# Kernel optimization log

Measured on AMD Instinct MI355X. Metric: run time of the kernel, lower is better.

Reference implementation:

```python
import jax, jax.numpy as jnp
import numpy as np

N_ATOMS = 50000
N_INT = 800000  # interactions (i,j pairs)
N_IN = 128
NFM = 128
LOG2 = float(np.log(2.0))


def ssp(a):
    # shifted softplus: log(0.5*exp(x) + 0.5) = softplus(x) - log(2)
    return jax.nn.softplus(a) - LOG2


def setup_inputs() -> dict:
    key = jax.random.key(0)
    ks = jax.random.split(key, 12)
    s = 1.0 / np.sqrt(NFM)
    inp = {
        "x": jax.random.normal(ks[0], (N_ATOMS, NFM), dtype=jnp.float32),
        "dijk": jax.random.normal(ks[1], (N_INT, N_IN), dtype=jnp.float32),
        "idx_j": jax.random.randint(ks[2], (N_INT,), 0, N_ATOMS),
        "seg_i": jnp.sort(jax.random.randint(ks[3], (N_INT,), 0, N_ATOMS)),
        "seg_j": jnp.arange(N_INT),
        "seg_i_sum": jnp.ones((N_ATOMS,), dtype=jnp.int64 if jax.config.jax_enable_x64 else jnp.int32),
        # filternet params
        "W_f1": jax.random.normal(ks[4], (N_IN, NFM), dtype=jnp.float32) * s,
        "b_f1": jnp.zeros((NFM,), dtype=jnp.float32),
        "W_f2": jax.random.normal(ks[5], (NFM, NFM), dtype=jnp.float32) * s,
        "b_f2": jnp.zeros((NFM,), dtype=jnp.float32),
        # cfconv params
        "W_in2fac": jax.random.normal(ks[6], (NFM, NFM), dtype=jnp.float32) * s,
        "W_fac2out": jax.random.normal(ks[7], (NFM, NFM), dtype=jnp.float32) * s,
        "b_fac2out": jnp.zeros((NFM,), dtype=jnp.float32),
        # output dense params
        "W_dense": jax.random.normal(ks[8], (NFM, NFM), dtype=jnp.float32) * s,
        "b_dense": jnp.zeros((NFM,), dtype=jnp.float32),
    }
    return inp


def reference(x, dijk, idx_j, seg_i, seg_j, seg_i_sum,
              W_f1, b_f1, W_f2, b_f2,
              W_in2fac, W_fac2out, b_fac2out,
              W_dense, b_dense):
    n_atoms = x.shape[0]
    n_int = idx_j.shape[0]
    # CFnetFilter: two shifted-softplus dense layers over triples, pool -> per-interaction filters
    h = ssp(dijk @ W_f1 + b_f1)                                   # [T, nFM]
    w_ijk = ssp(h @ W_f2 + b_f2)                                  # [T, nFM]
    w_ij = jax.ops.segment_sum(w_ijk, seg_j, num_segments=n_int)  # [E, nFM]
    # CFConv: in2fac dense, gather neighbor features, filter-multiply, segment-sum pool, fac2out dense
    f = x @ W_in2fac                                              # [N, nFM]
    f_j = f[idx_j]                                                # gather -> [E, nFM]
    wf = w_ij * f_j                                               # [E, nFM]
    conv = jax.ops.segment_sum(wf, seg_i, num_segments=n_atoms)   # [N, nFM]
    c = ssp(conv @ W_fac2out + b_fac2out)                         # [N, nFM]
    # output dense (no activation) + residual
    v = c @ W_dense + b_dense                                     # [N, nFM]
    y = x + v
    return (y, v)
```

## Files before the change

kernel.cpp:

```cpp
#include <hip/hip_runtime.h>
#include <hip/hip_bf16.h>
#include <stdint.h>

#define NATOMS 50000
#define NINT   800000
#define NFM    128
#define VOFF   (NATOMS*NFM)
#define NBLK   (NINT/256)
#define CBLK   (NINT/128)

typedef __bf16 bf16x8 __attribute__((ext_vector_type(8)));
typedef float  f32x4  __attribute__((ext_vector_type(4)));
typedef unsigned short u16;
typedef u16 u16x8 __attribute__((ext_vector_type(8)));
typedef u16 u16x4 __attribute__((ext_vector_type(4)));

__device__ __forceinline__ u16 f2b(float f){
  __bf16 h = (__bf16)f;
  return __builtin_bit_cast(u16, h);
}
__device__ __forceinline__ float b2f(u16 v){
  return (float)__builtin_bit_cast(__bf16, v);
}

__device__ __forceinline__ float sspf(float x){
  float t = exp2f(-fabsf(x) * 1.44269504088896f);
  return fmaxf(x, 0.0f) + 0.69314718055995f * log2f(1.0f + t) - 0.69314718055995f;
}

__global__ void zero_k(float4* __restrict__ p, int n4){
  int i = blockIdx.x * blockDim.x + threadIdx.x;
  int stride = gridDim.x * blockDim.x;
  float4 z = make_float4(0.f, 0.f, 0.f, 0.f);
  for (; i < n4; i += stride) p[i] = z;
}

__global__ void prep_weights_k(const float* __restrict__ w0, const float* __restrict__ w1,
                               const float* __restrict__ w2, const float* __restrict__ w3,
                               const float* __restrict__ w4, u16* __restrict__ wt){
  const float* srcs[5] = {w0, w1, w2, w3, w4};
  const float* src = srcs[blockIdx.x];
  u16* dst = wt + (size_t)blockIdx.x * NFM * NFM;
  for (int i = threadIdx.x; i < NFM*NFM; i += blockDim.x){
    int n = i >> 7, k = i & 127;
    dst[i] = f2b(src[k*NFM + n]);
  }
}

__device__ __forceinline__ void stage_inp(u16* lsA, const float* __restrict__ src,
                                          int base_row, int n_total, int t){
  #pragma unroll
  for (int pp = 0; pp < 8; ++pp){
    int id  = pp*512 + t;
    int row = id >> 4, c = id & 15;
    int grow = base_row + row;
    float4 v0 = make_float4(0.f,0.f,0.f,0.f), v1 = v0;
    if (grow < n_total){
      const float4* gp = reinterpret_cast<const float4*>(src + (size_t)grow*NFM + c*8);
      v0 = gp[0]; v1 = gp[1];
    }
    u16x8 pk;
    pk[0]=f2b(v0.x); pk[1]=f2b(v0.y); pk[2]=f2b(v0.z); pk[3]=f2b(v0.w);
    pk[4]=f2b(v1.x); pk[5]=f2b(v1.y); pk[6]=f2b(v1.z); pk[7]=f2b(v1.w);
    int byte = row*256 + ((c*16) ^ ((row & 7) << 4));
    *reinterpret_cast<u16x8*>(reinterpret_cast<char*>(lsA) + byte) = pk;
  }
}

__device__ __forceinline__ void stage_w(u16* lsW, const u16* __restrict__ wt, int t){
  #pragma unroll
  for (int pp = 0; pp < 4; ++pp){
    int id = pp*512 + t;
    int n = id >> 4, c = id & 15;
    u16x8 v = *reinterpret_cast<const u16x8*>(wt + n*NFM + c*8);
    int byte = n*256 + ((c*16) ^ ((n & 7) << 4));
    *reinterpret_cast<u16x8*>(reinterpret_cast<char*>(lsW) + byte) = v;
  }
}

__device__ __forceinline__ void gemm_tile(const u16* lsA, const u16* lsW,
                                          int wrow, int l15, int lk, f32x4 acc[2][8]){
  #pragma unroll
  for (int ks = 0; ks < 4; ++ks){
    int kb2 = (ks*32 + lk*8) * 2;
    int r0 = wrow + l15, r1 = wrow + 16 + l15;
    bf16x8 a0 = *reinterpret_cast<const bf16x8*>(reinterpret_cast<const char*>(lsA) + r0*256 + (kb2 ^ ((r0 & 7) << 4)));
    bf16x8 a1 = *reinterpret_cast<const bf16x8*>(reinterpret_cast<const char*>(lsA) + r1*256 + (kb2 ^ ((r1 & 7) << 4)));
    #pragma unroll
    for (int ni = 0; ni < 8; ++ni){
      int n = ni*16 + l15;
      bf16x8 b = *reinterpret_cast<const bf16x8*>(reinterpret_cast<const char*>(lsW) + n*256 + (kb2 ^ ((n & 7) << 4)));
      acc[0][ni] = __builtin_amdgcn_mfma_f32_16x16x32_bf16(a0, b, acc[0][ni], 0, 0, 0);
      acc[1][ni] = __builtin_amdgcn_mfma_f32_16x16x32_bf16(a1, b, acc[1][ni], 0, 0, 0);
    }
  }
}

__global__ __launch_bounds__(512, 2) void in2fac_k(const float* __restrict__ x,
                                                   const u16* __restrict__ wt,
                                                   u16* __restrict__ f_g){
  __shared__ u16 lsA[256*128];
  __shared__ u16 lsW[128*128];
  int t = threadIdx.x;
  int B0 = blockIdx.x * 256;
  stage_inp(lsA, x, B0, NATOMS, t);
  stage_w(lsW, wt, t);
  __syncthreads();
  int wid = t >> 6, lane = t & 63, l15 = lane & 15, lk = lane >> 4;
  int wrow = wid * 32;
  f32x4 acc[2][8] = {};
  gemm_tile(lsA, lsW, wrow, l15, lk, acc);
  #pragma unroll
  for (int mi = 0; mi < 2; ++mi)
    #pragma unroll
    for (int ni = 0; ni < 8; ++ni)
      #pragma unroll
      for (int j = 0; j < 4; ++j){
        int grow = B0 + wrow + mi*16 + lk*4 + j;
        if (grow < NATOMS) f_g[(size_t)grow*NFM + ni*16 + l15] = f2b(acc[mi][ni][j]);
      }
}

__global__ __launch_bounds__(512) __attribute__((amdgpu_waves_per_eu(4, 4)))
void filter_k(const float* __restrict__ dijk,
              const float* __restrict__ b_f1, const float* __restrict__ b_f2,
              const u16* __restrict__ wt1, const u16* __restrict__ wt2,
              u16* __restrict__ w_g){
  __shared__ u16 lsW[2*128*128];
  __shared__ u16 lsS[8192];
  int t = threadIdx.x;
  int B0 = blockIdx.x * 256;
  int wid = t >> 6, lane = t & 63, l15 = lane & 15, lk = lane >> 4;

  f32x4 araw[16];
  {
    const float* abase = dijk + (size_t)(B0 + wid*32 + l15) * NFM;
    #pragma unroll
    for (int mi = 0; mi < 2; ++mi)
      #pragma unroll
      for (int ks = 0; ks < 4; ++ks){
        const f32x4* gp = reinterpret_cast<const f32x4*>(abase + mi*16*NFM + ks*32 + lk*8);
        araw[(mi*4+ks)*2+0] = __builtin_nontemporal_load(gp);
        araw[(mi*4+ks)*2+1] = __builtin_nontemporal_load(gp+1);
      }
  }

  stage_w(lsW, wt1, t);
  stage_w(lsW + 16384, wt2, t);

  float bias1[8], bias2[8];
  #pragma unroll
  for (int ni = 0; ni < 8; ++ni){ bias1[ni] = b_f1[ni*16 + l15]; bias2[ni] = b_f2[ni*16 + l15]; }

  bf16x8 aa[2][4];
  #pragma unroll
  for (int mi = 0; mi < 2; ++mi)
    #pragma unroll
    for (int ks = 0; ks < 4; ++ks){
      f32x4 v0 = araw[(mi*4+ks)*2], v1 = araw[(mi*4+ks)*2+1];
      u16x8 pk;
      pk[0]=f2b(v0[0]); pk[1]=f2b(v0[1]); pk[2]=f2b(v0[2]); pk[3]=f2b(v0[3]);
      pk[4]=f2b(v1[0]); pk[5]=f2b(v1[1]); pk[6]=f2b(v1[2]); pk[7]=f2b(v1[3]);
      aa[mi][ks] = __builtin_bit_cast(bf16x8, pk);
    }

  __syncthreads();

  char* wbase = reinterpret_cast<char*>(lsS) + wid*2048;
  const char* lsW1b = reinterpret_cast<const char*>(lsW);
  const char* lsW2b = reinterpret_cast<const char*>(lsW + 16384);

  #pragma unroll
  for (int mi = 0; mi < 2; ++mi){
    f32x4 acc[8] = {};
    #pragma unroll
    for (int ks = 0; ks < 4; ++ks){
      int kb2 = (ks*32 + lk*8) * 2;
      #pragma unroll
      for (int ni = 0; ni < 8; ++ni){
        int n = ni*16 + l15;
        bf16x8 b = *reinterpret_cast<const bf16x8*>(lsW1b + n*256 + (kb2 ^ ((n & 7) << 4)));
        acc[ni] = __builtin_amdgcn_mfma_f32_16x16x32_bf16(aa[mi][ks], b, acc[ni], 0, 0, 0);
      }
    }
    bf16x8 h[4];
    #pragma unroll
    for (int p = 0; p < 2; ++p){
      #pragma unroll
      for (int nn = 0; nn < 4; ++nn){
        int col = nn*16 + l15;
        #pragma unroll
        for (int j = 0; j < 4; ++j){
          int r = lk*4 + j;
          *reinterpret_cast<u16*>(wbase + r*128 + ((col*2) ^ ((r & 7) << 4))) = f2b(sspf(acc[p*4+nn][j] + bias1[p*4+nn]));
        }
      }
      #pragma unroll
      for (int ksl = 0; ksl < 2; ++ksl)
        h[p*2+ksl] = *reinterpret_cast<const bf16x8*>(wbase + l15*128 + ((ksl*64 + lk*16) ^ ((l15 & 7) << 4)));
    }
    #pragma unroll
    for (int p = 0; p < 2; ++p){
      f32x4 acc2[4] = {};
      #pragma unroll
      for (int ks = 0; ks < 4; ++ks){
        int kb2 = (ks*32 + lk*8) * 2;
        #pragma unroll
        for (int nn = 0; nn < 4; ++nn){
          int n = (p*4 + nn)*16 + l15;
          bf16x8 b = *reinterpret_cast<const bf16x8*>(lsW2b + n*256 + (kb2 ^ ((n & 7) << 4)));
          acc2[nn] = __builtin_amdgcn_mfma_f32_16x16x32_bf16(h[ks], b, acc2[nn], 0, 0, 0);
        }
      }
      #pragma unroll
      for (int nn = 0; nn < 4; ++nn){
        int col = nn*16 + l15;
        #pragma unroll
        for (int j = 0; j < 4; ++j){
          int r = lk*4 + j;
          *reinterpret_cast<u16*>(wbase + r*128 + ((col*2) ^ ((r & 7) << 4))) = f2b(sspf(acc2[nn][j] + bias2[p*4+nn]));
        }
      }
      int row16 = lane & 15, chunk = lane >> 4;
      u16x8 v0 = *reinterpret_cast<const u16x8*>(wbase + row16*128 + ((chunk*32) ^ ((row16 & 7) << 4)));
      u16x8 v1 = *reinterpret_cast<const u16x8*>(wbase + row16*128 + ((chunk*32 + 16) ^ ((row16 & 7) << 4)));
      u16* gdst = w_g + (size_t)(B0 + wid*32 + mi*16 + row16)*NFM + p*64 + chunk*16;
      *reinterpret_cast<u16x8*>(gdst)     = v0;
      *reinterpret_cast<u16x8*>(gdst + 8) = v1;
    }
  }
}

__global__ __launch_bounds__(512) void conv_k(const int* __restrict__ idx_j,
    const int* __restrict__ seg_i, const u16* __restrict__ f_g,
    const u16* __restrict__ w_g, float* __restrict__ conv){
  __shared__ int lsSeg[128];
  __shared__ int lsIdx[128];
  int t = threadIdx.x;
  int B0 = blockIdx.x * 128;
  if (t < 128){ lsSeg[t] = seg_i[B0 + t]; lsIdx[t] = idx_j[B0 + t]; }
  __syncthreads();
  int c2 = t & 63, q = t >> 6;
  int qs = q*16, qe = qs + 16;
  int gc = c2*2;
  int prevseg = (qs > 0) ? lsSeg[qs-1] : (B0 > 0 ? seg_i[B0-1] : -1);
  int nextseg = (qe < 128) ? lsSeg[qe] : (B0 + 128 < NINT ? seg_i[B0+128] : -1);
  const u16* wtile = w_g + (size_t)B0*NFM;
  float s0 = 0.f, s1 = 0.f;
  int cur = lsSeg[qs], rs = qs;
  #pragma unroll 8
  for (int r = qs; r < qe; ++r){
    int sg = lsSeg[r];
    uint32_t wv = __builtin_nontemporal_load(reinterpret_cast<const uint32_t*>(wtile + (size_t)r*NFM + gc));
    uint32_t fv = *reinterpret_cast<const uint32_t*>(f_g + (size_t)lsIdx[r]*NFM + gc);
    if (sg != cur){
      float* dp = conv + (size_t)cur*NFM + gc;
      if (rs == qs && prevseg == cur){ atomicAdd(dp, s0); atomicAdd(dp+1, s1); }
      else { *reinterpret_cast<float2*>(dp) = make_float2(s0, s1); }
      cur = sg; rs = r; s0 = 0.f; s1 = 0.f;
    }
    s0 = fmaf(b2f((u16)(wv & 0xffff)), b2f((u16)(fv & 0xffff)), s0);
    s1 = fmaf(b2f((u16)(wv >> 16)),   b2f((u16)(fv >> 16)),   s1);
  }
  float* dp = conv + (size_t)cur*NFM + gc;
  if ((rs == qs && prevseg == cur) || nextseg == cur){ atomicAdd(dp, s0); atomicAdd(dp+1, s1); }
  else { *reinterpret_cast<float2*>(dp) = make_float2(s0, s1); }
}

__global__ __launch_bounds__(512, 2) void out_k(const float* __restrict__ conv,
    const float* __restrict__ x, const u16* __restrict__ wt3, const u16* __restrict__ wt4,
    const float* __restrict__ b3, const float* __restrict__ b4, float* __restrict__ out){
  __shared__ u16 lsA[256*128];
  __shared__ u16 lsW1[128*128];
  __shared__ u16 lsW2[128*128];
  int t = threadIdx.x;
  int B0 = blockIdx.x * 256;
  stage_inp(lsA, conv, B0, NATOMS, t);
  stage_w(lsW1, wt3, t);
  stage_w(lsW2, wt4, t);
  __syncthreads();
  int wid = t >> 6, lane = t & 63, l15 = lane & 15, lk = lane >> 4;
  int wrow = wid * 32;
  float bias3[8], bias4[8];
  #pragma unroll
  for (int ni = 0; ni < 8; ++ni){ bias3[ni] = b3[ni*16 + l15]; bias4[ni] = b4[ni*16 + l15]; }

  f32x4 acc1[2][8] = {};
  gemm_tile(lsA, lsW1, wrow, l15, lk, acc1);
  #pragma unroll
  for (int mi = 0; mi < 2; ++mi)
    #pragma unroll
    for (int ni = 0; ni < 8; ++ni)
      #pragma unroll
      for (int j = 0; j < 4; ++j){
        int row = wrow + mi*16 + lk*4 + j;
        int col = ni*16 + l15;
        u16 hb = f2b(sspf(acc1[mi][ni][j] + bias3[ni]));
        int byte = row*256 + ((col*2) ^ ((row & 7) << 4));
        *reinterpret_cast<u16*>(reinterpret_cast<char*>(lsA) + byte) = hb;
      }

  f32x4 acc2[2][8] = {};
  gemm_tile(lsA, lsW2, wrow, l15, lk, acc2);
  #pragma unroll
  for (int mi = 0; mi < 2; ++mi)
    #pragma unroll
    for (int ni = 0; ni < 8; ++ni)
      #pragma unroll
      for (int j = 0; j < 4; ++j){
        int grow = B0 + wrow + mi*16 + lk*4 + j;
        if (grow < NATOMS){
          int col = ni*16 + l15;
          float v = acc2[mi][ni][j] + bias4[ni];
          float yv = x[(size_t)grow*NFM + col] + v;
          out[(size_t)grow*NFM + col] = yv;
          out[(size_t)VOFF + (size_t)grow*NFM + col] = v;
        }
      }
}

extern "C" void kernel_launch(void* const* d_in, const int* in_sizes, int n_in,
                              void* d_out, int out_size, void* d_ws, size_t ws_size,
                              hipStream_t stream){
  const float* x        = (const float*)d_in[0];
  const float* dijk     = (const float*)d_in[1];
  const int*   idx_j    = (const int*)d_in[2];
  const int*   seg_i    = (const int*)d_in[3];
  const float* W_f1     = (const float*)d_in[6];
  const float* b_f1     = (const float*)d_in[7];
  const float* W_f2     = (const float*)d_in[8];
  const float* b_f2     = (const float*)d_in[9];
  const float* W_in2fac = (const float*)d_in[10];
  const float* W_fac2o  = (const float*)d_in[11];
  const float* b_fac2o  = (const float*)d_in[12];
  const float* W_dense  = (const float*)d_in[13];
  const float* b_dense  = (const float*)d_in[14];
  float* out = (float*)d_out;

  char* ws = (char*)d_ws;
  u16*   f_g  = (u16*)ws;
  float* conv = (float*)(ws + 12800000);
  u16*   wt   = (u16*)(ws + 38400000);
  u16*   w_g  = (u16*)(ws + 38600000);
  u16* wt1 = wt;
  u16* wt2 = wt + 16384;
  u16* wt5 = wt + 2*16384;
  u16* wt3 = wt + 3*16384;
  u16* wt4 = wt + 4*16384;

  prep_weights_k<<<5, 256, 0, stream>>>(W_f1, W_f2, W_in2fac, W_fac2o, W_dense, wt);
  zero_k<<<2048, 256, 0, stream>>>(reinterpret_cast<float4*>(conv), NATOMS*NFM/4);
  in2fac_k<<<(NATOMS + 255)/256, 512, 0, stream>>>(x, wt5, f_g);
  filter_k<<<NBLK, 512, 0, stream>>>(dijk, b_f1, b_f2, wt1, wt2, w_g);
  conv_k<<<CBLK, 512, 0, stream>>>(idx_j, seg_i, f_g, w_g, conv);
  out_k<<<(NATOMS + 255)/256, 512, 0, stream>>>(conv, x, wt3, wt4, b_fac2o, b_dense, out);
}
```

Before: 328.1 us.

## Widen conv blocks to 512 rows with one column per thread, simplify softplus

The conv kernel now gives each block 512 interactions, each thread one column over 128 consecutive rows instead of two columns over 16 rows. Longer per-thread row runs should mean fewer boundary atomics and fewer blocks. The cost is narrower 2-byte loads instead of 4-byte ones and less parallelism per row. The shifted softplus also drops its numerically stable form for a direct log(1+exp(x)), which is cheaper but can overflow for large positive inputs.

```diff
diff --git a/kernel.cpp b/kernel.cpp
--- a/kernel.cpp
+++ b/kernel.cpp
@@ -7,7 +7,8 @@
 #define NFM    128
 #define VOFF   (NATOMS*NFM)
 #define NBLK   (NINT/256)
-#define CBLK   (NINT/128)
+#define CVROWS 512
+#define CVBLK  ((NINT + CVROWS - 1)/CVROWS)
 
 typedef __bf16 bf16x8 __attribute__((ext_vector_type(8)));
 typedef float  f32x4  __attribute__((ext_vector_type(4)));
@@ -24,8 +25,8 @@
 }
 
 __device__ __forceinline__ float sspf(float x){
-  float t = exp2f(-fabsf(x) * 1.44269504088896f);
-  return fmaxf(x, 0.0f) + 0.69314718055995f * log2f(1.0f + t) - 0.69314718055995f;
+  float t = exp2f(x * 1.44269504088896f);
+  return 0.69314718055995f * (log2f(1.0f + t) - 1.0f);
 }
 
 __global__ void zero_k(float4* __restrict__ p, int n4){
@@ -234,37 +235,36 @@
 __global__ __launch_bounds__(512) void conv_k(const int* __restrict__ idx_j,
     const int* __restrict__ seg_i, const u16* __restrict__ f_g,
     const u16* __restrict__ w_g, float* __restrict__ conv){
-  __shared__ int lsSeg[128];
-  __shared__ int lsIdx[128];
+  __shared__ int lsSeg[CVROWS];
+  __shared__ int lsIdx[CVROWS];
   int t = threadIdx.x;
-  int B0 = blockIdx.x * 128;
-  if (t < 128){ lsSeg[t] = seg_i[B0 + t]; lsIdx[t] = idx_j[B0 + t]; }
+  int B0 = blockIdx.x * CVROWS;
+  int navail = NINT - B0; if (navail > CVROWS) navail = CVROWS;
+  if (t < navail){ lsSeg[t] = seg_i[B0 + t]; lsIdx[t] = idx_j[B0 + t]; }
   __syncthreads();
-  int c2 = t & 63, q = t >> 6;
-  int qs = q*16, qe = qs + 16;
-  int gc = c2*2;
+  int col = t & 127, q = t >> 7;
+  int qs = q*128;
+  if (qs >= navail) return;
+  int qe = qs + 128; if (qe > navail) qe = navail;
   int prevseg = (qs > 0) ? lsSeg[qs-1] : (B0 > 0 ? seg_i[B0-1] : -1);
-  int nextseg = (qe < 128) ? lsSeg[qe] : (B0 + 128 < NINT ? seg_i[B0+128] : -1);
+  int nextseg = (qe < navail) ? lsSeg[qe] : (B0 + qe < NINT ? seg_i[B0+qe] : -1);
   const u16* wtile = w_g + (size_t)B0*NFM;
-  float s0 = 0.f, s1 = 0.f;
+  float s = 0.f;
   int cur = lsSeg[qs], rs = qs;
   #pragma unroll 8
   for (int r = qs; r < qe; ++r){
     int sg = lsSeg[r];
-    uint32_t wv = __builtin_nontemporal_load(reinterpret_cast<const uint32_t*>(wtile + (size_t)r*NFM + gc));
-    uint32_t fv = *reinterpret_cast<const uint32_t*>(f_g + (size_t)lsIdx[r]*NFM + gc);
+    float wv = b2f(wtile[(size_t)r*NFM + col]);
+    float fv = b2f(f_g[(size_t)lsIdx[r]*NFM + col]);
     if (sg != cur){
-      float* dp = conv + (size_t)cur*NFM + gc;
-      if (rs == qs && prevseg == cur){ atomicAdd(dp, s0); atomicAdd(dp+1, s1); }
-      else { *reinterpret_cast<float2*>(dp) = make_float2(s0, s1); }
-      cur = sg; rs = r; s0 = 0.f; s1 = 0.f;
-    }
-    s0 = fmaf(b2f((u16)(wv & 0xffff)), b2f((u16)(fv & 0xffff)), s0);
-    s1 = fmaf(b2f((u16)(wv >> 16)),   b2f((u16)(fv >> 16)),   s1);
-  }
-  float* dp = conv + (size_t)cur*NFM + gc;
-  if ((rs == qs && prevseg == cur) || nextseg == cur){ atomicAdd(dp, s0); atomicAdd(dp+1, s1); }
-  else { *reinterpret_cast<float2*>(dp) = make_float2(s0, s1); }
+      float* dp = conv + (size_t)cur*NFM + col;
+      if (rs == qs && prevseg == cur) atomicAdd(dp, s); else *dp = s;
+      cur = sg; rs = r; s = 0.f;
+    }
+    s = fmaf(wv, fv, s);
+  }
+  float* dp = conv + (size_t)cur*NFM + col;
+  if ((rs == qs && prevseg == cur) || nextseg == cur) atomicAdd(dp, s); else *dp = s;
 }
 
 __global__ __launch_bounds__(512, 2) void out_k(const float* __restrict__ conv,
@@ -352,6 +352,6 @@
   zero_k<<<2048, 256, 0, stream>>>(reinterpret_cast<float4*>(conv), NATOMS*NFM/4);
   in2fac_k<<<(NATOMS + 255)/256, 512, 0, stream>>>(x, wt5, f_g);
   filter_k<<<NBLK, 512, 0, stream>>>(dijk, b_f1, b_f2, wt1, wt2, w_g);
-  conv_k<<<CBLK, 512, 0, stream>>>(idx_j, seg_i, f_g, w_g, conv);
+  conv_k<<<CVBLK, 512, 0, stream>>>(idx_j, seg_i, f_g, w_g, conv);
   out_k<<<(NATOMS + 255)/256, 512, 0, stream>>>(conv, x, wt3, wt4, b_fac2o, b_dense, out);
 }
```

New measurement: 326.5 us. Within noise of the previous version (-0.5%).
